# Kernel optimization log

Hardware: AMD Instinct MI355X
Metric: run time of the kernel (lower is better)

Reference implementation:

```python
import jax, jax.numpy as jnp
import numpy as np

# DCNv3Bottleneck(c1=256, c2=256, shortcut=True, g=4, e=0.5, kernel_size=3)
N, C1, C2, H, W = 8, 256, 256, 56, 56
CMID = 128                      # c_ = int(c2 * e)
G, KS, PAD, DIL, STRIDE = 4, 3, 1, 1, 1
K2 = KS * KS                    # 9 sampling points
EPS = 1e-5


def conv2d(x, w, stride=1, pad=0, groups=1):
    return jax.lax.conv_general_dilated(
        x, w, (stride, stride), [(pad, pad), (pad, pad)],
        feature_group_count=groups,
        dimension_numbers=('NCHW', 'OIHW', 'NCHW'))


def bn(x, g, b, m, v):  # inference BatchNorm2d, NCHW
    inv = jax.lax.rsqrt(v + EPS)
    return x * (g * inv).reshape(1, -1, 1, 1) + (b - m * g * inv).reshape(1, -1, 1, 1)


def layernorm(x, g, b):  # over last (channel) axis
    mu = x.mean(-1, keepdims=True)
    var = x.var(-1, keepdims=True)
    return (x - mu) * jax.lax.rsqrt(var + EPS) * g + b


def bilinear_sample(v, loc):
    """grid_sample(bilinear, zeros padding, align_corners=False).
    v: (N,G,Hp,Wp,gc) values; loc: (N,G,L,K2,2) normalized (x,y) in [-1,1].
    returns (N,G,L,K2,gc)."""
    n, g, hp, wp, gc = v.shape
    x = (loc[..., 0] + 1) * wp / 2 - 0.5
    y = (loc[..., 1] + 1) * hp / 2 - 0.5
    x0 = jnp.floor(x)
    y0 = jnp.floor(y)
    wx1 = x - x0
    wy1 = y - y0
    x0i = x0.astype(jnp.int32)
    y0i = y0.astype(jnp.int32)
    vf = v.reshape(n, g, hp * wp, gc)

    def gather(yi, xi):
        valid = (yi >= 0) & (yi < hp) & (xi >= 0) & (xi < wp)
        idx = jnp.clip(yi, 0, hp - 1) * wp + jnp.clip(xi, 0, wp - 1)
        out = jnp.take_along_axis(vf, idx.reshape(n, g, -1, 1), axis=2)
        return out.reshape(*idx.shape, gc) * valid[..., None]

    return (gather(y0i, x0i) * ((1 - wy1) * (1 - wx1))[..., None]
            + gather(y0i, x0i + 1) * ((1 - wy1) * wx1)[..., None]
            + gather(y0i + 1, x0i) * (wy1 * (1 - wx1))[..., None]
            + gather(y0i + 1, x0i + 1) * (wy1 * wx1)[..., None])


def dcnv3_core(value, offset, mask):
    """InternImage dcnv3_core_pytorch, offset_scale=1.0.
    value: (N,H,W,C) NHWC; offset: (N,H,W,G*K2*2); mask: (N,H,W,G,K2) softmaxed."""
    n, h, w, c = value.shape
    gc = c // G
    v = jnp.pad(value, ((0, 0), (PAD, PAD), (PAD, PAD), (0, 0)))
    hp, wp = h + 2 * PAD, w + 2 * PAD
    hout, wout = h, w  # stride 1, same padding
    # reference points (centers of output locations), normalized by padded dims
    start = DIL * (KS - 1) / 2 + 0.5
    ry = (start + jnp.arange(hout) * STRIDE) / hp
    rx = (start + jnp.arange(wout) * STRIDE) / wp
    ref = jnp.stack(jnp.meshgrid(rx, ry, indexing='xy'), -1)  # (Hout,Wout,2) = (x,y)
    # dilation kernel grid
    base = -((DIL * (KS - 1)) // 2)
    px = (base + jnp.arange(KS) * DIL) / wp
    py = (base + jnp.arange(KS) * DIL) / hp
    gx, gy = jnp.meshgrid(px, py, indexing='ij')
    kgrid = jnp.stack([gx, gy], -1).reshape(K2, 2)
    # sampling locations: shared base grid per group + learned per-group offsets
    base_loc = ref[None, :, :, None, :] + kgrid[None, None, None, :, :]  # (1,H,W,K2,2)
    off = offset.reshape(n, hout, wout, G, K2, 2) / jnp.array([wp, hp], value.dtype)
    samp = base_loc[:, :, :, None, :, :] + off                           # (N,H,W,G,K2,2)
    grid = (2 * samp - 1).reshape(n, hout * wout, G, K2, 2).transpose(0, 2, 1, 3, 4)
    vg = v.reshape(n, hp, wp, G, gc).transpose(0, 3, 1, 2, 4)            # (N,G,Hp,Wp,gc)
    sampled = bilinear_sample(vg, grid)                                  # (N,G,L,K2,gc)
    m = mask.reshape(n, hout * wout, G, K2).transpose(0, 2, 1, 3)        # (N,G,L,K2)
    out = jnp.einsum('nglk,nglkc->nglc', m, sampled)
    return out.transpose(0, 2, 1, 3).reshape(n, hout, wout, c)


def _forward(x, w_cv1, bn1_g, bn1_b, bn1_m, bn1_v,
             w_dw, b_dw, ln_g, ln_b, w_inp, b_inp,
             w_off, b_off, w_msk, b_msk, w_out, b_out,
             bn2_g, bn2_b, bn2_m, bn2_v):
    # cv1: 3x3 conv -> BN -> SiLU
    h = jax.nn.silu(bn(conv2d(x, w_cv1, 1, 1), bn1_g, bn1_b, bn1_m, bn1_v))  # (N,CMID,H,W)
    # offset/mask branch: depthwise 3x3 -> LN (channels_last) -> GELU
    t = conv2d(h, w_dw, 1, (KS - 1) // 2, groups=CMID) + b_dw.reshape(1, -1, 1, 1)
    t = jax.nn.gelu(layernorm(t.transpose(0, 2, 3, 1), ln_g, ln_b), approximate=False)
    xh = h.transpose(0, 2, 3, 1)                       # NHWC
    value = xh @ w_inp + b_inp                         # input_proj
    offset = t @ w_off + b_off                         # (N,H,W,G*K2*2), shared per group
    mask = jax.nn.softmax((t @ w_msk + b_msk).reshape(*t.shape[:3], G, K2), axis=-1)
    o = dcnv3_core(value, offset, mask)
    o = (o @ w_out + b_out).transpose(0, 3, 1, 2)      # output_proj c_ -> c2, back to NCHW
    o = jax.nn.silu(bn(o, bn2_g, bn2_b, bn2_m, bn2_v))
    return x + o                                       # shortcut (c1 == c2)


def setup_inputs() -> dict:
    key = jax.random.key(0)
    ks = jax.random.split(key, 8)
    rn = lambda k, s, sc=0.02: jax.random.normal(k, s, jnp.float32) * sc
    return {
        'x': jax.random.normal(ks[0], (N, C1, H, W), jnp.float32),
        'w_cv1': rn(ks[1], (CMID, C1, 3, 3)),
        'bn1_g': jnp.ones((CMID,), jnp.float32), 'bn1_b': jnp.zeros((CMID,), jnp.float32),
        'bn1_m': jnp.zeros((CMID,), jnp.float32), 'bn1_v': jnp.ones((CMID,), jnp.float32),
        'w_dw': rn(ks[2], (CMID, 1, KS, KS)), 'b_dw': jnp.zeros((CMID,), jnp.float32),
        'ln_g': jnp.ones((CMID,), jnp.float32), 'ln_b': jnp.zeros((CMID,), jnp.float32),
        'w_inp': rn(ks[3], (CMID, CMID)), 'b_inp': jnp.zeros((CMID,), jnp.float32),
        'w_off': rn(ks[4], (CMID, G * K2 * 2), 0.01), 'b_off': jnp.zeros((G * K2 * 2,), jnp.float32),
        'w_msk': rn(ks[5], (CMID, G * K2), 0.01), 'b_msk': jnp.zeros((G * K2,), jnp.float32),
        'w_out': rn(ks[6], (CMID, C2)), 'b_out': jnp.zeros((C2,), jnp.float32),
        'bn2_g': jnp.ones((C2,), jnp.float32), 'bn2_b': jnp.zeros((C2,), jnp.float32),
        'bn2_m': jnp.zeros((C2,), jnp.float32), 'bn2_v': jnp.ones((C2,), jnp.float32),
    }


def reference(x, w_cv1, bn1_g, bn1_b, bn1_m, bn1_v,
              w_dw, b_dw, ln_g, ln_b, w_inp, b_inp,
              w_off, b_off, w_msk, b_msk, w_out, b_out,
              bn2_g, bn2_b, bn2_m, bn2_v):
    return _forward(x, w_cv1, bn1_g, bn1_b, bn1_m, bn1_v,
                    w_dw, b_dw, ln_g, ln_b, w_inp, b_inp,
                    w_off, b_off, w_msk, b_msk, w_out, b_out,
                    bn2_g, bn2_b, bn2_m, bn2_v)
```

## Files before the change

### kernel.cpp

```cpp
#include <hip/hip_runtime.h>
#include <hip/hip_bf16.h>

typedef __hip_bfloat16 bf16;
typedef float f32x4 __attribute__((ext_vector_type(4)));
typedef short s16x8 __attribute__((ext_vector_type(8)));

#define NN 8
#define HH 56
#define WW 56
#define C1 256
#define CM 128
#define C2 256
#define GG 4
#define K2K 9
#define HWSZ (HH*WW)
#define LL (NN*HWSZ)
#define EPSF 1e-5f
#define XP_H 58
#define XP_W 58

__device__ __forceinline__ float b2f(bf16 v){ return __bfloat162float(v); }

__global__ __launch_bounds__(256) void k0pre(
    const float* __restrict__ x, const float* __restrict__ w,
    const float* __restrict__ wout, const float* __restrict__ winp,
    const float* __restrict__ woff, const float* __restrict__ wmsk,
    const float* __restrict__ g2, const float* __restrict__ bb2,
    const float* __restrict__ m2, const float* __restrict__ v2,
    const float* __restrict__ bout, const float* __restrict__ wdw,
    bf16* __restrict__ xp, bf16* __restrict__ Wf, bf16* __restrict__ Wf2,
    bf16* __restrict__ Wf3, bf16* __restrict__ Wf4,
    float* __restrict__ scbi, float* __restrict__ wdwT)
{
    int bidg = blockIdx.x;
    if (bidg < 1856){
        __shared__ float lds[64][57];
        int n = bidg / 232; int rem = bidg % 232;
        int yp = rem >> 2; int ci0 = (rem & 3) << 6;
        int tid = threadIdx.x;
        bool interior = (yp >= 1 && yp <= 56);
        if (interior){
            int y = yp - 1;
            for (int e = tid; e < 64*56; e += 256){
                int ci = e / 56, xx = e - (e/56)*56;
                lds[ci][xx] = x[((size_t)((n*C1 + ci0 + ci)*HH) + y)*WW + xx];
            }
            __syncthreads();
        }
        for (int g = tid; g < 464; g += 256){
            int pxp = g >> 3, cig = (g & 7) << 3;
            s16x8 v;
            if (!interior || pxp == 0 || pxp == 57){
                #pragma unroll
                for (int j=0;j<8;j++) ((bf16*)&v)[j] = __float2bfloat16(0.f);
            } else {
                #pragma unroll
                for (int j=0;j<8;j++) ((bf16*)&v)[j] = __float2bfloat16(lds[cig+j][pxp-1]);
            }
            *(s16x8*)(xp + ((size_t)(n*XP_H + yp)*XP_W + pxp)*C1 + ci0 + cig) = v;
        }
        return;
    }
    if (bidg < 2000){
        int tlin = (bidg-1856)*256 + threadIdx.x;
        int kt  = tlin >> 9;
        int rem = tlin & 511;
        int nt  = rem >> 6;
        int lane = rem & 63;
        int co = nt*16 + (lane & 15);
        int kbase = kt*32 + (lane >> 4)*8;
        bf16* dst = Wf + (size_t)tlin*8;
        #pragma unroll
        for (int j = 0; j < 8; j++){
            int k = kbase + j;
            int tap = k >> 8;
            int ci  = k & 255;
            dst[j] = __float2bfloat16(w[((size_t)co*C1 + ci)*9 + tap]);
        }
        return;
    }
    int t = (bidg-2000)*256 + threadIdx.x;
    if (t < 4096){
        int lane = t & 63; int kc = (t>>6)&3; int mt = t>>8;
        int co = mt*16 + (lane&15); int k0 = kc*32 + (lane>>4)*8;
        bf16* d = Wf2 + (size_t)t*8;
        #pragma unroll
        for (int j=0;j<8;j++) d[j] = __float2bfloat16(wout[(size_t)(k0+j)*C2 + co]);
    } else if (t < 6144){
        int u = t - 4096; int lane = u&63; int kc=(u>>6)&3; int nt=u>>8;
        int co = nt*16+(lane&15); int k0 = kc*32+(lane>>4)*8;
        bf16* d = Wf3 + (size_t)u*8;
        #pragma unroll
        for (int j=0;j<8;j++) d[j] = __float2bfloat16(winp[(size_t)(k0+j)*CM + co]);
    } else if (t < 7936){
        int u = t - 6144; int lane=u&63; int kc=(u>>6)&3; int nt=u>>8;
        int nn2 = nt*16+(lane&15); int k0 = kc*32+(lane>>4)*8;
        bf16* d = Wf4 + (size_t)u*8;
        #pragma unroll
        for (int j=0;j<8;j++){
            int k = k0+j; float v = 0.f;
            if (nn2 < 72) v = woff[(size_t)k*72 + nn2];
            else if (nn2 < 108) v = wmsk[(size_t)k*36 + (nn2-72)];
            d[j] = __float2bfloat16(v);
        }
    } else if (t < 8192){
        int co = t - 7936;
        float sc = g2[co]*rsqrtf(v2[co]+EPSF);
        scbi[co] = sc;
        scbi[256+co] = bb2[co] - m2[co]*sc + bout[co]*sc;
    } else if (t < 8192 + 9*CM){
        int u = t - 8192;
        int tap = u >> 7, c = u & 127;
        wdwT[tap*CM + c] = wdw[c*9 + tap];
    }
}

__device__ __forceinline__ void stageB(const bf16* __restrict__ Wf, int s, bf16* buf, int w, int lane){
    const bf16* g = Wf + ((size_t)s << 12) + (w << 10) + lane*8;
    bf16* l = buf + (w << 10);
    __builtin_amdgcn_global_load_lds((const __attribute__((address_space(1))) void*)g,
                                     (__attribute__((address_space(3))) void*)l, 16, 0, 0);
    __builtin_amdgcn_global_load_lds((const __attribute__((address_space(1))) void*)(g + 512),
                                     (__attribute__((address_space(3))) void*)(l + 512), 16, 0, 0);
}

__device__ __forceinline__ s16x8 loadA1(const bf16* __restrict__ xp, long abase, int s){
    int tap = s >> 3; int dy = tap/3, dx = tap - dy*3;
    int off = ((dy-1)*XP_W + (dx-1))*C1 + ((s&7)<<5);
    return *(const s16x8*)(xp + abase + off);
}

__global__ __launch_bounds__(256) void k1_mfma(
    const bf16* __restrict__ xp, const bf16* __restrict__ Wf,
    const float* __restrict__ bg, const float* __restrict__ bb,
    const float* __restrict__ bm, const float* __restrict__ bv,
    bf16* __restrict__ hb)
{
    __shared__ __align__(16) bf16 Bbuf[2][8192];
    int bid = blockIdx.x;
    int n = bid/98, p0 = (bid%98)*32;
    int tid = threadIdx.x, lane = tid & 63;
    int w  = tid >> 6;
    int wm = w & 1, wn = w >> 1;
    int kpart = lane >> 4;
    int col = lane & 15;
    int pxA = p0 + wm*16 + col;
    int yA = pxA/WW, xxA = pxA - yA*WW;
    long abase = ((long)((n*XP_H + yA + 1)*XP_W) + (xxA+1))*C1 + kpart*8;

    f32x4 acc[4] = {{0,0,0,0},{0,0,0,0},{0,0,0,0},{0,0,0,0}};

    stageB(Wf, 0, &Bbuf[0][0],    w, lane);
    stageB(Wf, 1, &Bbuf[0][4096], w, lane);
    s16x8 A0 = loadA1(xp, abase, 0);
    s16x8 A1 = loadA1(xp, abase, 1);
    __syncthreads();

    for (int ss = 0; ss < 36; ++ss){
        s16x8 An0 = A0, An1 = A1;
        if (ss + 1 < 36){
            stageB(Wf, 2*ss+2, &Bbuf[(ss+1)&1][0],    w, lane);
            stageB(Wf, 2*ss+3, &Bbuf[(ss+1)&1][4096], w, lane);
            An0 = loadA1(xp, abase, 2*ss+2);
            An1 = loadA1(xp, abase, 2*ss+3);
        }
        const bf16* bufp = &Bbuf[ss&1][0] + (wn << 11) + lane*8;
        #pragma unroll
        for (int ct = 0; ct < 4; ++ct){
            s16x8 bfrag = *(const s16x8*)(bufp + (ct << 9));
            acc[ct] = __builtin_amdgcn_mfma_f32_16x16x32_bf16(A0, bfrag, acc[ct], 0, 0, 0);
        }
        #pragma unroll
        for (int ct = 0; ct < 4; ++ct){
            s16x8 bfrag = *(const s16x8*)(bufp + 4096 + (ct << 9));
            acc[ct] = __builtin_amdgcn_mfma_f32_16x16x32_bf16(A1, bfrag, acc[ct], 0, 0, 0);
        }
        __syncthreads();
        A0 = An0; A1 = An1;
    }

    int pxO = p0 + wm*16 + kpart*4;
    #pragma unroll
    for (int ct = 0; ct < 4; ++ct){
        int co = (wn << 6) + (ct << 4) + col;
        float sc = bg[co] * rsqrtf(bv[co] + EPSF);
        float bi = bb[co] - bm[co]*sc;
        #pragma unroll
        for (int r = 0; r < 4; ++r){
            int px = pxO + r;
            float z = acc[ct][r]*sc + bi;
            float sl = z / (1.f + expf(-z));
            hb[((size_t)n*HWSZ + px)*CM + co] = __float2bfloat16(sl);
        }
    }
}

__global__ __launch_bounds__(128) void k2v(
    const bf16* __restrict__ hb, const float* __restrict__ wdwT, const float* __restrict__ bdw,
    const float* __restrict__ lng, const float* __restrict__ lnb, bf16* __restrict__ tb)
{
    int t = threadIdx.x;
    int p = t >> 4, s = t & 15;
    int pix = blockIdx.x*8 + p;
    int n = pix / HWSZ, rem = pix % HWSZ;
    int y = rem / WW, xq = rem % WW;
    int c0 = s*8;
    const bf16* hbase = hb + (size_t)n*HWSZ*CM;
    float acc[8];
    {
        float4 b0 = *(const float4*)(bdw + c0);
        float4 b1 = *(const float4*)(bdw + c0 + 4);
        acc[0]=b0.x; acc[1]=b0.y; acc[2]=b0.z; acc[3]=b0.w;
        acc[4]=b1.x; acc[5]=b1.y; acc[6]=b1.z; acc[7]=b1.w;
    }
    #pragma unroll
    for (int tap=0; tap<9; tap++){
        int dy=tap/3, dx=tap%3;
        int yy=y+dy-1, xx=xq+dx-1;
        if ((unsigned)yy < HH && (unsigned)xx < WW){
            s16x8 v = *(const s16x8*)(hbase + ((size_t)(yy*WW+xx))*CM + c0);
            float4 w0 = *(const float4*)(wdwT + tap*CM + c0);
            float4 w1 = *(const float4*)(wdwT + tap*CM + c0 + 4);
            float wv[8] = {w0.x,w0.y,w0.z,w0.w,w1.x,w1.y,w1.z,w1.w};
            #pragma unroll
            for (int j=0;j<8;j++)
                acc[j] += b2f(((bf16*)&v)[j]) * wv[j];
        }
    }
    float s1=0.f, s2=0.f;
    #pragma unroll
    for (int j=0;j<8;j++){ s1 += acc[j]; s2 += acc[j]*acc[j]; }
    #pragma unroll
    for (int off=1; off<16; off<<=1){
        s1 += __shfl_xor(s1, off);
        s2 += __shfl_xor(s2, off);
    }
    float mean = s1*(1.f/CM);
    float var  = fmaxf(s2*(1.f/CM) - mean*mean, 0.f);
    float inv  = rsqrtf(var + EPSF);
    float4 g0 = *(const float4*)(lng + c0); float4 g1 = *(const float4*)(lng + c0+4);
    float4 q0 = *(const float4*)(lnb + c0); float4 q1 = *(const float4*)(lnb + c0+4);
    float gv[8]={g0.x,g0.y,g0.z,g0.w,g1.x,g1.y,g1.z,g1.w};
    float qv[8]={q0.x,q0.y,q0.z,q0.w,q1.x,q1.y,q1.z,q1.w};
    s16x8 ov;
    #pragma unroll
    for (int j=0;j<8;j++){
        float z = (acc[j]-mean)*inv*gv[j] + qv[j];
        float gl = 0.5f*z*(1.f + erff(z*0.70710678118654752f));
        ((bf16*)&ov)[j] = __float2bfloat16(gl);
    }
    *(s16x8*)(tb + (size_t)pix*CM + c0) = ov;
}

__global__ __launch_bounds__(256) void k3_gemm(
    const bf16* __restrict__ hb, const bf16* __restrict__ tb,
    const bf16* __restrict__ Wf3, const bf16* __restrict__ Wf4,
    const float* __restrict__ binp, const float* __restrict__ boff, const float* __restrict__ bmsk,
    bf16* __restrict__ val, float* __restrict__ om)
{
    __shared__ __align__(16) bf16 Ah[32*136];
    __shared__ __align__(16) bf16 At[32*136];
    int blk = blockIdx.x;
    int n = blk/98; int p0 = (blk%98)*32;
    size_t pixbase = (size_t)n*HWSZ + p0;
    int tid = threadIdx.x;
    for (int e = tid; e < 512; e += 256){
        int row = e>>4, seg = e&15;
        *(s16x8*)&Ah[row*136 + seg*8] = *(const s16x8*)(hb + (pixbase+row)*CM + seg*8);
        *(s16x8*)&At[row*136 + seg*8] = *(const s16x8*)(tb + (pixbase+row)*CM + seg*8);
    }
    __syncthreads();
    int lane = tid & 63, w = tid >> 6;
    int col = lane & 15, kq = lane >> 4;
    int mt = w & 1, wn = w >> 1;
    s16x8 a0[4], a1[4];
    #pragma unroll
    for (int kc=0;kc<4;kc++){
        a0[kc] = *(const s16x8*)&Ah[(mt*16+col)*136 + kc*32 + kq*8];
        a1[kc] = *(const s16x8*)&At[(mt*16+col)*136 + kc*32 + kq*8];
    }
    int pxo = p0 + mt*16 + kq*4;
    #pragma unroll
    for (int nti=0; nti<4; nti++){
        int nt = wn*4 + nti;
        f32x4 acc = {0,0,0,0};
        #pragma unroll
        for (int kc=0;kc<4;kc++){
            s16x8 b = *(const s16x8*)(Wf3 + ((size_t)(nt*4+kc)*64 + lane)*8);
            acc = __builtin_amdgcn_mfma_f32_16x16x32_bf16(a0[kc], b, acc, 0, 0, 0);
        }
        int co = nt*16 + col;
        float bia = binp[co];
        #pragma unroll
        for (int r=0;r<4;r++)
            val[((size_t)n*HWSZ + pxo + r)*CM + co] = __float2bfloat16(acc[r] + bia);
    }
    #pragma unroll
    for (int nti=0; nti<4; nti++){
        int nt = wn*4 + nti;
        if (nt < 7){
            f32x4 acc = {0,0,0,0};
            #pragma unroll
            for (int kc=0;kc<4;kc++){
                s16x8 b = *(const s16x8*)(Wf4 + ((size_t)(nt*4+kc)*64 + lane)*8);
                acc = __builtin_amdgcn_mfma_f32_16x16x32_bf16(a1[kc], b, acc, 0, 0, 0);
            }
            int nn2 = nt*16 + col;
            float bia = (nn2<72) ? boff[nn2] : (nn2<108 ? bmsk[nn2-72] : 0.f);
            #pragma unroll
            for (int r=0;r<4;r++)
                om[((size_t)n*HWSZ + pxo + r)*112 + nn2] = acc[r] + bia;
        }
    }
}

__global__ __launch_bounds__(128) void k4a(
    const bf16* __restrict__ valb, const float* __restrict__ om, bf16* __restrict__ o)
{
    __shared__ float omb[8][112];
    __shared__ float mk[8][36];
    int t = threadIdx.x;
    int pix0 = blockIdx.x*8;
    for (int e = t; e < 8*112; e += 128){
        int p = e / 112, q = e - (e/112)*112;
        omb[p][q] = om[(size_t)(pix0+p)*112 + q];
    }
    __syncthreads();
    if (t < 32){
        int p = t >> 2, g = t & 3;
        float mx = omb[p][72+g*9];
        #pragma unroll
        for (int j=1;j<9;j++) mx = fmaxf(mx, omb[p][72+g*9+j]);
        float sum=0.f; float e9[9];
        #pragma unroll
        for (int j=0;j<9;j++){ e9[j] = expf(omb[p][72+g*9+j]-mx); sum += e9[j]; }
        float inv = 1.f/sum;
        #pragma unroll
        for (int j=0;j<9;j++) mk[p][g*9+j] = e9[j]*inv;
    }
    __syncthreads();
    int p = t >> 4, s = t & 15;
    int g = s >> 2;
    int c0 = s*8;
    int pix = pix0 + p;
    int n = pix / HWSZ, rem = pix % HWSZ;
    int y = rem / WW, xq = rem % WW;
    const bf16* vb = valb + (size_t)n*HWSZ*CM;
    float acc[8] = {0,0,0,0,0,0,0,0};
    #pragma unroll
    for (int k=0;k<9;k++){
        float oxv = omb[p][g*18 + k*2];
        float oyv = omb[p][g*18 + k*2 + 1];
        float sx = (float)xq + (float)(k/3) - 1.f + oxv;
        float sy = (float)y  + (float)(k%3) - 1.f + oyv;
        float x0f = floorf(sx), y0f = floorf(sy);
        float fx = sx - x0f, fy = sy - y0f;
        int x0 = (int)x0f, y0 = (int)y0f;
        float mw = mk[p][g*9+k];
        float w00 = (1.f-fy)*(1.f-fx)*mw;
        float w01 = (1.f-fy)*fx*mw;
        float w10 = fy*(1.f-fx)*mw;
        float w11 = fy*fx*mw;
        if ((unsigned)y0 < HH && (unsigned)x0 < WW){
            s16x8 v = *(const s16x8*)(vb + ((size_t)(y0*WW+x0))*CM + c0);
            #pragma unroll
            for (int j=0;j<8;j++) acc[j] += w00*b2f(((bf16*)&v)[j]);
        }
        if ((unsigned)y0 < HH && (unsigned)(x0+1) < WW){
            s16x8 v = *(const s16x8*)(vb + ((size_t)(y0*WW+x0+1))*CM + c0);
            #pragma unroll
            for (int j=0;j<8;j++) acc[j] += w01*b2f(((bf16*)&v)[j]);
        }
        if ((unsigned)(y0+1) < HH && (unsigned)x0 < WW){
            s16x8 v = *(const s16x8*)(vb + ((size_t)((y0+1)*WW+x0))*CM + c0);
            #pragma unroll
            for (int j=0;j<8;j++) acc[j] += w10*b2f(((bf16*)&v)[j]);
        }
        if ((unsigned)(y0+1) < HH && (unsigned)(x0+1) < WW){
            s16x8 v = *(const s16x8*)(vb + ((size_t)((y0+1)*WW+x0+1))*CM + c0);
            #pragma unroll
            for (int j=0;j<8;j++) acc[j] += w11*b2f(((bf16*)&v)[j]);
        }
    }
    s16x8 ov;
    #pragma unroll
    for (int j=0;j<8;j++) ((bf16*)&ov)[j] = __float2bfloat16(acc[j]);
    *(s16x8*)(o + (size_t)pix*CM + c0) = ov;
}

__global__ __launch_bounds__(256) void k4b(
    const bf16* __restrict__ o, const bf16* __restrict__ Wf2, const float* __restrict__ scbi,
    const float* __restrict__ xin, float* __restrict__ out)
{
    __shared__ __align__(16) bf16 Bl[64*136];
    int blk = blockIdx.x;
    int n = blk/49; int p0 = (blk%49)*64;
    int tid = threadIdx.x;
    for (int e = tid; e < 1024; e += 256){
        int row = e>>4, seg = e&15;
        *(s16x8*)&Bl[row*136 + seg*8] = *(const s16x8*)(o + ((size_t)n*HWSZ + p0 + row)*CM + seg*8);
    }
    __syncthreads();
    int lane = tid & 63, w = tid >> 6;
    int col = lane & 15, kq = lane >> 4;
    int co0 = w*64;
    s16x8 af[4][4];
    #pragma unroll
    for (int mt=0;mt<4;mt++)
        #pragma unroll
        for (int kc=0;kc<4;kc++)
            af[mt][kc] = *(const s16x8*)(Wf2 + (((size_t)((co0>>4)+mt)*4 + kc)*64 + lane)*8);
    f32x4 acc[4][4];
    #pragma unroll
    for (int mt=0;mt<4;mt++)
        #pragma unroll
        for (int nt=0;nt<4;nt++)
            acc[mt][nt] = (f32x4){0,0,0,0};
    #pragma unroll
    for (int nt=0;nt<4;nt++){
        s16x8 bfr[4];
        #pragma unroll
        for (int kc=0;kc<4;kc++)
            bfr[kc] = *(const s16x8*)&Bl[(nt*16+col)*136 + kc*32 + kq*8];
        #pragma unroll
        for (int mt=0;mt<4;mt++)
            #pragma unroll
            for (int kc=0;kc<4;kc++)
                acc[mt][nt] = __builtin_amdgcn_mfma_f32_16x16x32_bf16(af[mt][kc], bfr[kc], acc[mt][nt], 0, 0, 0);
    }
    #pragma unroll
    for (int mt=0;mt<4;mt++){
        #pragma unroll
        for (int r=0;r<4;r++){
            int co = co0 + mt*16 + kq*4 + r;
            float sc = scbi[co], bi = scbi[256+co];
            #pragma unroll
            for (int nt=0;nt<4;nt++){
                int px = p0 + nt*16 + col;
                size_t idx = ((size_t)(n*C2 + co))*HWSZ + px;
                float z = acc[mt][nt][r]*sc + bi;
                float sl = z/(1.f+expf(-z));
                out[idx] = sl + xin[idx];
            }
        }
    }
}

extern "C" void kernel_launch(void* const* d_in, const int* in_sizes, int n_in,
                              void* d_out, int out_size, void* d_ws, size_t ws_size,
                              hipStream_t stream)
{
    const float* x    = (const float*)d_in[0];
    const float* wcv1 = (const float*)d_in[1];
    const float* bn1g = (const float*)d_in[2];
    const float* bn1b = (const float*)d_in[3];
    const float* bn1m = (const float*)d_in[4];
    const float* bn1v = (const float*)d_in[5];
    const float* wdw  = (const float*)d_in[6];
    const float* bdw  = (const float*)d_in[7];
    const float* lng  = (const float*)d_in[8];
    const float* lnb  = (const float*)d_in[9];
    const float* winp = (const float*)d_in[10];
    const float* binp = (const float*)d_in[11];
    const float* woff = (const float*)d_in[12];
    const float* boff = (const float*)d_in[13];
    const float* wmsk = (const float*)d_in[14];
    const float* bmsk = (const float*)d_in[15];
    const float* wout = (const float*)d_in[16];
    const float* bout = (const float*)d_in[17];
    const float* bn2g = (const float*)d_in[18];
    const float* bn2b = (const float*)d_in[19];
    const float* bn2m = (const float*)d_in[20];
    const float* bn2v = (const float*)d_in[21];

    unsigned char* base = (unsigned char*)d_ws;
    bf16*  Wf   = (bf16*)(base);
    bf16*  Wf2  = (bf16*)(base + 589824);
    bf16*  Wf3  = (bf16*)(base + 655360);
    bf16*  Wf4  = (bf16*)(base + 688128);
    float* scbi = (float*)(base + 716800);
    float* wdwT = (float*)(base + 718848);
    bf16*  xp   = (bf16*)(base + 723456);
    bf16*  tb   = (bf16*)(base + 723456);
    bf16*  val  = (bf16*)(base + 7145984);
    bf16*  hb   = (bf16*)(base + 14502400);
    float* om   = (float*)(base + 20924928);
    bf16*  o    = (bf16*)(base + 32164352);

    hipLaunchKernelGGL(k0pre, dim3(2037), dim3(256), 0, stream,
                       x, wcv1, wout, winp, woff, wmsk, bn2g, bn2b, bn2m, bn2v, bout, wdw,
                       xp, Wf, Wf2, Wf3, Wf4, scbi, wdwT);
    hipLaunchKernelGGL(k1_mfma, dim3(NN*98), dim3(256), 0, stream,
                       xp, Wf, bn1g, bn1b, bn1m, bn1v, hb);
    hipLaunchKernelGGL(k2v, dim3(LL/8), dim3(128), 0, stream,
                       hb, wdwT, bdw, lng, lnb, tb);
    hipLaunchKernelGGL(k3_gemm, dim3(NN*98), dim3(256), 0, stream,
                       hb, tb, Wf3, Wf4, binp, boff, bmsk, val, om);
    hipLaunchKernelGGL(k4a, dim3(LL/8), dim3(128), 0, stream, val, om, o);
    hipLaunchKernelGGL(k4b, dim3(NN*49), dim3(256), 0, stream, o, Wf2, scbi, x, (float*)d_out);
}
```

Measured before the change: 231.3 us.

## Stage A tiles through swizzled LDS and retile k1 warps to 2x2 MFMA blocks

The 3x3 conv GEMM in k1 now loads its activation (A) fragments into a double-buffered, XOR-swizzled LDS buffer with global_load_lds, no longer reading them per lane straight from global memory into registers. The warp tiling changes so each wave covers all 32 pixels and 32 output channels, using 2x2 MFMA tiles that reuse each A and B fragment twice. The aim is to cut duplicated global A reads and to overlap A loads with compute the same way B loads already are. The cost is extra LDS traffic and footprint per block, and it relies on the swizzle being bank-conflict free and correct.

```diff
diff --git a/kernel.cpp b/kernel.cpp
--- a/kernel.cpp
+++ b/kernel.cpp
@@ -115,8 +115,8 @@
     }
 }
 
-__device__ __forceinline__ void stageB(const bf16* __restrict__ Wf, int s, bf16* buf, int w, int lane){
-    const bf16* g = Wf + ((size_t)s << 12) + (w << 10) + lane*8;
+__device__ __forceinline__ void stageB(const bf16* __restrict__ Wf, int s32, bf16* buf, int w, int lane){
+    const bf16* g = Wf + ((size_t)s32 << 12) + (w << 10) + lane*8;
     bf16* l = buf + (w << 10);
     __builtin_amdgcn_global_load_lds((const __attribute__((address_space(1))) void*)g,
                                      (__attribute__((address_space(3))) void*)l, 16, 0, 0);
@@ -124,12 +124,6 @@
                                      (__attribute__((address_space(3))) void*)(l + 512), 16, 0, 0);
 }
 
-__device__ __forceinline__ s16x8 loadA1(const bf16* __restrict__ xp, long abase, int s){
-    int tap = s >> 3; int dy = tap/3, dx = tap - dy*3;
-    int off = ((dy-1)*XP_W + (dx-1))*C1 + ((s&7)<<5);
-    return *(const s16x8*)(xp + abase + off);
-}
-
 __global__ __launch_bounds__(256) void k1_mfma(
     const bf16* __restrict__ xp, const bf16* __restrict__ Wf,
     const float* __restrict__ bg, const float* __restrict__ bb,
@@ -137,60 +131,76 @@
     bf16* __restrict__ hb)
 {
     __shared__ __align__(16) bf16 Bbuf[2][8192];
+    __shared__ __align__(16) bf16 Abuf[2][2048];
     int bid = blockIdx.x;
     int n = bid/98, p0 = (bid%98)*32;
     int tid = threadIdx.x, lane = tid & 63;
     int w  = tid >> 6;
-    int wm = w & 1, wn = w >> 1;
-    int kpart = lane >> 4;
-    int col = lane & 15;
-    int pxA = p0 + wm*16 + col;
-    int yA = pxA/WW, xxA = pxA - yA*WW;
-    long abase = ((long)((n*XP_H + yA + 1)*XP_W) + (xxA+1))*C1 + kpart*8;
-
-    f32x4 acc[4] = {{0,0,0,0},{0,0,0,0},{0,0,0,0},{0,0,0,0}};
-
-    stageB(Wf, 0, &Bbuf[0][0],    w, lane);
-    stageB(Wf, 1, &Bbuf[0][4096], w, lane);
-    s16x8 A0 = loadA1(xp, abase, 0);
-    s16x8 A1 = loadA1(xp, abase, 1);
+    int col = lane & 15, kq = lane >> 4;
+
+    int pS = tid >> 3;
+    int gS = ((tid & 7) + pS) & 7;
+    {
+    }
+    int pxS = p0 + pS;
+    int yS = pxS/WW, xS = pxS - yS*WW;
+    long sbase = ((long)((n*XP_H + yS + 1)*XP_W) + (xS + 1))*C1 + gS*8;
+
+    int sw0 = (kq - col) & 7;
+    int sw1 = (kq + 4 - col) & 7;
+
+    f32x4 acc[2][2];
+    #pragma unroll
+    for (int mi=0;mi<2;mi++)
+        #pragma unroll
+        for (int ct=0;ct<2;ct++) acc[mi][ct] = (f32x4){0,0,0,0};
+
+    #define STAGE(s, b) do { \
+        stageB(Wf, 2*(s),   &Bbuf[b][0],    w, lane); \
+        stageB(Wf, 2*(s)+1, &Bbuf[b][4096], w, lane); \
+        int tap_ = (s) >> 2; int dy_ = tap_/3, dx_ = tap_ - dy_*3; \
+        int ci0_ = ((s) & 3) << 6; \
+        const bf16* ga_ = xp + sbase + ((dy_-1)*XP_W + (dx_-1))*C1 + ci0_; \
+        __builtin_amdgcn_global_load_lds((const __attribute__((address_space(1))) void*)ga_, \
+            (__attribute__((address_space(3))) void*)(&Abuf[b][0] + (w << 9)), 16, 0, 0); \
+    } while(0)
+
+    STAGE(0, 0);
     __syncthreads();
 
-    for (int ss = 0; ss < 36; ++ss){
-        s16x8 An0 = A0, An1 = A1;
-        if (ss + 1 < 36){
-            stageB(Wf, 2*ss+2, &Bbuf[(ss+1)&1][0],    w, lane);
-            stageB(Wf, 2*ss+3, &Bbuf[(ss+1)&1][4096], w, lane);
-            An0 = loadA1(xp, abase, 2*ss+2);
-            An1 = loadA1(xp, abase, 2*ss+3);
-        }
-        const bf16* bufp = &Bbuf[ss&1][0] + (wn << 11) + lane*8;
-        #pragma unroll
-        for (int ct = 0; ct < 4; ++ct){
-            s16x8 bfrag = *(const s16x8*)(bufp + (ct << 9));
-            acc[ct] = __builtin_amdgcn_mfma_f32_16x16x32_bf16(A0, bfrag, acc[ct], 0, 0, 0);
-        }
-        #pragma unroll
-        for (int ct = 0; ct < 4; ++ct){
-            s16x8 bfrag = *(const s16x8*)(bufp + 4096 + (ct << 9));
-            acc[ct] = __builtin_amdgcn_mfma_f32_16x16x32_bf16(A1, bfrag, acc[ct], 0, 0, 0);
+    for (int s = 0; s < 36; ++s){
+        int b = s & 1;
+        if (s + 1 < 36) STAGE(s+1, b^1);
+        #pragma unroll
+        for (int ks = 0; ks < 2; ++ks){
+            int swk = ks ? sw1 : sw0;
+            s16x8 a0 = *(const s16x8*)&Abuf[b][ (col*8      + swk) * 8 ];
+            s16x8 a1 = *(const s16x8*)&Abuf[b][ ((16+col)*8 + swk) * 8 ];
+            s16x8 b0 = *(const s16x8*)&Bbuf[b][ ks*4096 + (w*2+0)*512 + lane*8 ];
+            s16x8 b1 = *(const s16x8*)&Bbuf[b][ ks*4096 + (w*2+1)*512 + lane*8 ];
+            acc[0][0] = __builtin_amdgcn_mfma_f32_16x16x32_bf16(a0, b0, acc[0][0], 0, 0, 0);
+            acc[0][1] = __builtin_amdgcn_mfma_f32_16x16x32_bf16(a0, b1, acc[0][1], 0, 0, 0);
+            acc[1][0] = __builtin_amdgcn_mfma_f32_16x16x32_bf16(a1, b0, acc[1][0], 0, 0, 0);
+            acc[1][1] = __builtin_amdgcn_mfma_f32_16x16x32_bf16(a1, b1, acc[1][1], 0, 0, 0);
         }
         __syncthreads();
-        A0 = An0; A1 = An1;
-    }
-
-    int pxO = p0 + wm*16 + kpart*4;
-    #pragma unroll
-    for (int ct = 0; ct < 4; ++ct){
-        int co = (wn << 6) + (ct << 4) + col;
+    }
+    #undef STAGE
+
+    #pragma unroll
+    for (int ct = 0; ct < 2; ++ct){
+        int co = w*32 + ct*16 + col;
         float sc = bg[co] * rsqrtf(bv[co] + EPSF);
         float bi = bb[co] - bm[co]*sc;
         #pragma unroll
-        for (int r = 0; r < 4; ++r){
-            int px = pxO + r;
-            float z = acc[ct][r]*sc + bi;
-            float sl = z / (1.f + expf(-z));
-            hb[((size_t)n*HWSZ + px)*CM + co] = __float2bfloat16(sl);
+        for (int mi = 0; mi < 2; ++mi){
+            #pragma unroll
+            for (int r = 0; r < 4; ++r){
+                int px = p0 + mi*16 + kq*4 + r;
+                float z = acc[mi][ct][r]*sc + bi;
+                float sl = z / (1.f + expf(-z));
+                hb[((size_t)n*HWSZ + px)*CM + co] = __float2bfloat16(sl);
+            }
         }
     }
 }
```

Measured after the change: 206.4 us. 10.7% less time.
